# Optimization experiments

Hardware: AMD Instinct MI355X
Metric: run time of the kernel (lower is better)

Reference implementation:

```python
import jax, jax.numpy as jnp
import numpy as np

B, LQ, LK, D = 4, 2048, 2048, 1024
H = 16  # num_heads == num_kv_heads (only runnable config of the source module)
HD = D // H  # 64


def setup_inputs() -> dict:
    key = jax.random.key(0)
    ks = jax.random.split(key, 4)
    std = 0.02
    return {
        "x": jax.random.normal(ks[0], (B, LQ, D), dtype=jnp.float32),
        "text_input": jax.random.normal(ks[1], (B, LK, D), dtype=jnp.float32),
        "Wq": jax.random.normal(ks[2], (D, D), dtype=jnp.float32) * std,
        "bq": jnp.zeros((D,), dtype=jnp.float32),
        "Wkv": jax.random.normal(ks[3], (D, 2 * D), dtype=jnp.float32) * std,
        "bkv": jnp.zeros((2 * D,), dtype=jnp.float32),
    }


def reference(x, text_input, Wq, bq, Wkv, bkv):
    b, lq, d = x.shape
    lk = text_input.shape[1]
    # projections
    Q = x @ Wq + bq                       # [b, lq, d]
    KV = text_input @ Wkv + bkv           # [b, lk, 2d]
    K, V = jnp.split(KV, 2, axis=-1)      # [b, lk, d] each
    # split heads (num_kv_heads == num_heads, so repeat_interleave is identity)
    Q = Q.reshape(b, lq, H, HD)
    K = K.reshape(b, lk, H, HD)
    V = V.reshape(b, lk, H, HD)
    # scaled dot-product attention
    scale = 1.0 / jnp.sqrt(jnp.asarray(HD, dtype=Q.dtype))
    scores = jnp.einsum("bqhd,bkhd->bhqk", Q, K) * scale  # [b, H, lq, lk]
    attn = jax.nn.softmax(scores, axis=-1)
    out = jnp.einsum("bhqk,bkhd->bqhd", attn, V)          # [b, lq, H, HD]
    # dropout p=0.0 (eval) -> identity
    return out.reshape(b, lq, d)
```

## Files before the change

### kernel.cpp

```cpp
#include <hip/hip_runtime.h>
#include <hip/hip_bf16.h>


typedef unsigned short u16;
typedef unsigned int u32;

typedef __attribute__((ext_vector_type(8))) __bf16 bf16x8;
typedef __attribute__((ext_vector_type(2))) _Float16 f16x2;
typedef __attribute__((ext_vector_type(8))) _Float16 f16x8;
typedef __attribute__((ext_vector_type(4))) float f32x4;
typedef __attribute__((ext_vector_type(16))) float f32x16;
typedef __attribute__((ext_vector_type(4))) float f4;
typedef __attribute__((ext_vector_type(4))) unsigned short u16x4;

#define DEVI __device__ __forceinline__

DEVI u16 f2b(float f) {
  u32 u = __float_as_uint(f);
  return (u16)((u + 0x7fffu + ((u >> 16) & 1u)) >> 16);
}

DEVI u16 f2h(float f) {
  _Float16 h = (_Float16)f;
  return __builtin_bit_cast(u16, h);
}

DEVI f16x2 pk_f16(float a, float b) {
  return __builtin_bit_cast(f16x2, __builtin_amdgcn_cvt_pkrtz(a, b));
}

DEVI void gld_lds16(void* lds, const void* g) {
  __builtin_amdgcn_global_load_lds(
      (const __attribute__((address_space(1))) u32*)g,
      (__attribute__((address_space(3))) u32*)lds, 16, 0, 0);
}

__global__ __launch_bounds__(256) void k_prep(
    const float* __restrict__ x, const float* __restrict__ text,
    const float* __restrict__ Wq, const float* __restrict__ Wkv,
    u16* __restrict__ XB, u16* __restrict__ TB,
    u16* __restrict__ WQT, u16* __restrict__ WKVT) {
  __shared__ float tile[32][33];
  const int bid = blockIdx.x, tid = threadIdx.x;
  if (bid < 4096) {
    const float* in = (bid < 2048) ? x : text;
    u16* out = (bid < 2048) ? XB : TB;
    const int cb = (bid < 2048) ? bid : bid - 2048;
#pragma unroll
    for (int it = 0; it < 4; it++) {
      int i = cb * 256 + tid + it * 524288;
      f4 v = ((const f4*)in)[i];
      u16x4 o;
      o.x = f2b(v.x); o.y = f2b(v.y); o.z = f2b(v.z); o.w = f2b(v.w);
      ((u16x4*)out)[i] = o;
    }
  } else {
    const float* in;
    u16* out;
    int N, bx, by;
    if (bid < 5120) {
      int b2 = bid - 4096; in = Wq; out = WQT; N = 1024; bx = b2 & 31; by = b2 >> 5;
    } else {
      int b2 = bid - 5120; in = Wkv; out = WKVT; N = 2048; bx = b2 & 63; by = b2 >> 6;
    }
    const int K = 1024;
    const int n0 = bx * 32, k0 = by * 32;
    const int tx = tid & 31, ty = tid >> 5;
#pragma unroll
    for (int j = 0; j < 32; j += 8)
      tile[ty + j][tx] = in[(size_t)(k0 + ty + j) * N + n0 + tx];
    __syncthreads();
#pragma unroll
    for (int j = 0; j < 32; j += 8)
      out[(size_t)(n0 + ty + j) * K + k0 + tx] = f2b(tile[tx][ty + j]);
  }
}

__global__ __launch_bounds__(256) void k_gemm(
    const u16* __restrict__ XB, const u16* __restrict__ TB,
    const u16* __restrict__ WQT, const u16* __restrict__ WKVT,
    const float* __restrict__ bq, const float* __restrict__ bkv,
    u16* __restrict__ QG, u16* __restrict__ KG, u16* __restrict__ VG) {
  __shared__ alignas(16) char As[2][8192];
  __shared__ alignas(16) char Bs[2][8192];
  const int bid0 = blockIdx.x;
  const int bid = (bid0 & 7) * 192 + (bid0 >> 3);
  const int tid = threadIdx.x;
  const int w = tid >> 6, l = tid & 63;
  const int wr = w >> 1, wc = w & 1;

  const bool isQ = bid < 512;
  int nb, mb;
  const u16 *Aptr, *Bptr;
  const float* bias;
  if (isQ) {
    nb = bid & 7; mb = bid >> 3; Aptr = XB; Bptr = WQT; bias = bq;
  } else {
    int b2 = bid - 512; nb = b2 & 15; mb = b2 >> 4; Aptr = TB; Bptr = WKVT; bias = bkv;
  }
  const int m0 = mb << 7, n0 = nb << 7;

  u32 soff[2], doff[2];
#pragma unroll
  for (int i = 0; i < 2; i++) {
    u32 o = (u32)(i * 4096 + tid * 16);
    u32 row = o >> 6;
    soff[i] = row * 2048 + ((o & 63) ^ ((row & 3) << 4));
    doff[i] = o;
  }
  const char* Aorig = (const char*)Aptr + (size_t)m0 * 2048;
  const char* Borig = (const char*)Bptr + (size_t)n0 * 2048;

  f32x16 acc[2][2];
#pragma unroll
  for (int i = 0; i < 2; i++)
#pragma unroll
    for (int j = 0; j < 2; j++)
#pragma unroll
      for (int e = 0; e < 16; e++) acc[i][j][e] = 0.f;

  const u32 x3 = (u32)(l & 3);
  const u32 hi5 = (u32)(l >> 5);
  const u32 arow0 = (u32)(wr * 64 + (l & 31)) * 64;
  const u32 brow0 = (u32)(wc * 64 + (l & 31)) * 64;

#pragma unroll
  for (int i = 0; i < 2; i++) {
    gld_lds16(&As[0][doff[i]], Aorig + soff[i]);
    gld_lds16(&Bs[0][doff[i]], Borig + soff[i]);
  }
  __syncthreads();
  int buf = 0;
  for (int kt = 0; kt < 32; kt++) {
    if (kt < 31) {
#pragma unroll
      for (int i = 0; i < 2; i++) {
        gld_lds16(&As[buf ^ 1][doff[i]], Aorig + (u32)(kt + 1) * 64 + soff[i]);
        gld_lds16(&Bs[buf ^ 1][doff[i]], Borig + (u32)(kt + 1) * 64 + soff[i]);
      }
    }
    bf16x8 af[2][2], bfr[2][2];
#pragma unroll
    for (int i = 0; i < 2; i++)
#pragma unroll
      for (int h = 0; h < 2; h++) {
        const u32 co = (((u32)(2 * h) + hi5) ^ x3) << 4;
        af[i][h] = *(const bf16x8*)&As[buf][arow0 + (u32)i * 2048 + co];
        bfr[i][h] = *(const bf16x8*)&Bs[buf][brow0 + (u32)i * 2048 + co];
      }
#pragma unroll
    for (int i = 0; i < 2; i++)
#pragma unroll
      for (int j = 0; j < 2; j++)
#pragma unroll
        for (int h = 0; h < 2; h++)
          acc[i][j] = __builtin_amdgcn_mfma_f32_32x32x16_bf16(af[i][h], bfr[j][h], acc[i][j], 0, 0, 0);
    __syncthreads();
    buf ^= 1;
  }

#pragma unroll
  for (int i = 0; i < 2; i++)
#pragma unroll
    for (int j = 0; j < 2; j++) {
      const int n = n0 + wc * 64 + j * 32 + (l & 31);
      const float bv = bias[n];
#pragma unroll
      for (int rg = 0; rg < 4; rg++) {
        const int mbase = m0 + wr * 64 + i * 32 + rg * 8 + ((l >> 5) << 2);
        const int bb = mbase >> 11;
        const int mrow = mbase & 2047;
        float a0 = acc[i][j][rg * 4 + 0] + bv;
        float a1 = acc[i][j][rg * 4 + 1] + bv;
        float a2 = acc[i][j][rg * 4 + 2] + bv;
        float a3 = acc[i][j][rg * 4 + 3] + bv;
        if (isQ) {
          const int h = n >> 6, hd = n & 63;
          u16* dst = QG + ((((size_t)bb * 16 + h) * 2048 + mrow) << 6) + hd;
          dst[0] = f2b(a0 * 0.18033688011112042f);
          dst[64] = f2b(a1 * 0.18033688011112042f);
          dst[128] = f2b(a2 * 0.18033688011112042f);
          dst[192] = f2b(a3 * 0.18033688011112042f);
        } else if (n < 1024) {
          const int h = n >> 6, d = n & 63;
          char* base = (char*)KG + ((((size_t)bb * 16 + h) * 2048 + mrow) << 7);
          float av[4] = {a0, a1, a2, a3};
#pragma unroll
          for (int r = 0; r < 4; r++) {
            u32 off = (u32)r * 128 + (((u32)d * 2) ^ (((u32)(mrow + r) & 7) << 4));
            *(u16*)(base + off) = f2b(av[r]);
          }
        } else {
          const int nn = n - 1024;
          const int h = nn >> 6, hd = nn & 63;
          u16x4 pk;
          pk.x = f2h(a0); pk.y = f2h(a1); pk.z = f2h(a2); pk.w = f2h(a3);
          char* base = (char*)VG + (((size_t)bb * 16 + h) << 18);
          u32 off = ((u32)(mrow >> 6) << 13) + (((u32)(mrow >> 5) & 1) << 12) +
                    ((u32)(hd >> 4) << 10) + (((u32)(mrow >> 2) & 3) << 8) +
                    ((u32)(hd & 15) << 4) + (((u32)(mrow >> 4) & 1) << 3);
          *(u16x4*)(base + off) = pk;
        }
      }
    }
}

__global__ __launch_bounds__(256) void k_attn(
    const u16* __restrict__ QG, const u16* __restrict__ KG, const u16* __restrict__ VG,
    float* __restrict__ out) {
  __shared__ alignas(16) char Ks[2][8192];
  __shared__ alignas(16) char Vs[2][8192];
  const int tid = threadIdx.x, w = tid >> 6, l = tid & 63;
  const int g = l >> 4, q = l & 15;
  const int bid = blockIdx.x;
  const int orig = (bid & 7) * 128 + (bid >> 3);
  const int qt = orig & 15;
  const int hh = (orig >> 4) & 15;
  const int b = orig >> 8;
  const size_t bh = (size_t)b * 16 + hh;

  const int qrowA = qt * 128 + w * 16 + q;
  const int qrowB = qrowA + 64;

  const u16* QpA = QG + ((bh * 2048 + (size_t)qrowA) << 6) + (g << 3);
  const u16* QpB = QG + ((bh * 2048 + (size_t)qrowB) << 6) + (g << 3);
  const bf16x8 qf0a = *(const bf16x8*)QpA;
  const bf16x8 qf1a = *(const bf16x8*)(QpA + 32);
  const bf16x8 qf0b = *(const bf16x8*)QpB;
  const bf16x8 qf1b = *(const bf16x8*)(QpB + 32);

  const char* Kbase = (const char*)KG + (bh << 18);
  const char* Vbase = (const char*)VG + (bh << 18);

  f32x4 lsA = (f32x4){0.f, 0.f, 0.f, 0.f};
  f32x4 lsB = (f32x4){0.f, 0.f, 0.f, 0.f};
  f32x4 oa[4], ob4[4];
#pragma unroll
  for (int c = 0; c < 4; c++) {
    oa[c] = (f32x4){0.f, 0.f, 0.f, 0.f};
    ob4[c] = (f32x4){0.f, 0.f, 0.f, 0.f};
  }
  f16x8 ones8;
#pragma unroll
  for (int e = 0; e < 8; e++) ones8[e] = (_Float16)1.0f;

  gld_lds16(&Ks[0][tid * 16], Kbase + tid * 16);
  gld_lds16(&Ks[0][4096 + tid * 16], Kbase + 4096 + tid * 16);
  gld_lds16(&Vs[0][tid * 16], Vbase + tid * 16);
  gld_lds16(&Vs[0][4096 + tid * 16], Vbase + 4096 + tid * 16);
  __syncthreads();

  const u32 ksw = ((u32)(l & 7)) << 4;
  const u32 kro = ((u32)q) << 7;
  const u32 kin = ((u32)g) << 4;

  auto body = [&](int BUF, int kb) {
    if (kb < 31) {
      const char* kp = Kbase + (size_t)(kb + 1) * 8192 + tid * 16;
      const char* vp = Vbase + (size_t)(kb + 1) * 8192 + tid * 16;
      gld_lds16(&Ks[BUF ^ 1][tid * 16], kp);
      gld_lds16(&Ks[BUF ^ 1][4096 + tid * 16], kp + 4096);
      gld_lds16(&Vs[BUF ^ 1][tid * 16], vp);
      gld_lds16(&Vs[BUF ^ 1][4096 + tid * 16], vp + 4096);
    }
    f32x4 sa[4], sb[4];
    __builtin_amdgcn_s_setprio(1);
#pragma unroll
    for (int t = 0; t < 4; t++) {
      const char* kr = &Ks[BUF][kro + (u32)t * 2048];
      bf16x8 kf0 = *(const bf16x8*)(kr + (kin ^ ksw));
      bf16x8 kf1 = *(const bf16x8*)(kr + ((kin + 64) ^ ksw));
      f32x4 z = (f32x4){0.f, 0.f, 0.f, 0.f};
      sa[t] = __builtin_amdgcn_mfma_f32_16x16x32_bf16(kf0, qf0a, z, 0, 0, 0);
      sa[t] = __builtin_amdgcn_mfma_f32_16x16x32_bf16(kf1, qf1a, sa[t], 0, 0, 0);
      sb[t] = __builtin_amdgcn_mfma_f32_16x16x32_bf16(kf0, qf0b, z, 0, 0, 0);
      sb[t] = __builtin_amdgcn_mfma_f32_16x16x32_bf16(kf1, qf1b, sb[t], 0, 0, 0);
    }
    __builtin_amdgcn_s_setprio(0);

    float pA[4][4], pB[4][4];
#pragma unroll
    for (int t = 0; t < 4; t++)
#pragma unroll
      for (int r = 0; r < 4; r++) {
        pA[t][r] = __builtin_amdgcn_exp2f(sa[t][r]);
        pB[t][r] = __builtin_amdgcn_exp2f(sb[t][r]);
      }

    __builtin_amdgcn_s_setprio(1);
#pragma unroll
    for (int u = 0; u < 2; u++) {
      f16x2 a0 = pk_f16(pA[2 * u][0], pA[2 * u][1]);
      f16x2 a1 = pk_f16(pA[2 * u][2], pA[2 * u][3]);
      f16x2 a2 = pk_f16(pA[2 * u + 1][0], pA[2 * u + 1][1]);
      f16x2 a3 = pk_f16(pA[2 * u + 1][2], pA[2 * u + 1][3]);
      f16x8 pfa;
      pfa[0] = a0.x; pfa[1] = a0.y; pfa[2] = a1.x; pfa[3] = a1.y;
      pfa[4] = a2.x; pfa[5] = a2.y; pfa[6] = a3.x; pfa[7] = a3.y;
      f16x2 b0 = pk_f16(pB[2 * u][0], pB[2 * u][1]);
      f16x2 b1 = pk_f16(pB[2 * u][2], pB[2 * u][3]);
      f16x2 b2 = pk_f16(pB[2 * u + 1][0], pB[2 * u + 1][1]);
      f16x2 b3 = pk_f16(pB[2 * u + 1][2], pB[2 * u + 1][3]);
      f16x8 pfb;
      pfb[0] = b0.x; pfb[1] = b0.y; pfb[2] = b1.x; pfb[3] = b1.y;
      pfb[4] = b2.x; pfb[5] = b2.y; pfb[6] = b3.x; pfb[7] = b3.y;
      lsA = __builtin_amdgcn_mfma_f32_16x16x32_f16(ones8, pfa, lsA, 0, 0, 0);
      lsB = __builtin_amdgcn_mfma_f32_16x16x32_f16(ones8, pfb, lsB, 0, 0, 0);
#pragma unroll
      for (int c = 0; c < 4; c++) {
        f16x8 vf = *(const f16x8*)&Vs[BUF][(u32)u * 4096 + (u32)c * 1024 + (u32)l * 16];
        oa[c] = __builtin_amdgcn_mfma_f32_16x16x32_f16(vf, pfa, oa[c], 0, 0, 0);
        ob4[c] = __builtin_amdgcn_mfma_f32_16x16x32_f16(vf, pfb, ob4[c], 0, 0, 0);
      }
    }
    __builtin_amdgcn_s_setprio(0);
    __syncthreads();
  };

  for (int kb2 = 0; kb2 < 16; kb2++) {
    body(0, 2 * kb2);
    body(1, 2 * kb2 + 1);
  }

  const float invA = 1.0f / lsA.x;
  const float invB = 1.0f / lsB.x;
  float* obA = out + ((size_t)b * 2048 + (size_t)qrowA) * 1024 + hh * 64;
  float* obB = out + ((size_t)b * 2048 + (size_t)qrowB) * 1024 + hh * 64;
#pragma unroll
  for (int c = 0; c < 4; c++) {
    f32x4 va = oa[c] * invA;
    f32x4 vb2 = ob4[c] * invB;
    *(f32x4*)(obA + c * 16 + g * 4) = va;
    *(f32x4*)(obB + c * 16 + g * 4) = vb2;
  }
}

extern "C" void kernel_launch(void* const* d_in, const int* in_sizes, int n_in,
                              void* d_out, int out_size, void* d_ws, size_t ws_size,
                              hipStream_t stream) {
  const float* x = (const float*)d_in[0];
  const float* text = (const float*)d_in[1];
  const float* Wq = (const float*)d_in[2];
  const float* bq = (const float*)d_in[3];
  const float* Wkv = (const float*)d_in[4];
  const float* bkv = (const float*)d_in[5];
  float* out = (float*)d_out;
  char* ws = (char*)d_ws;

  const size_t MiB = 1u << 20;
  u16* XB = (u16*)(ws + 0 * MiB);
  u16* TB = (u16*)(ws + 16 * MiB);
  u16* WQT = (u16*)(ws + 32 * MiB);
  u16* WKVT = (u16*)(ws + 34 * MiB);
  u16* QG = (u16*)(ws + 38 * MiB);
  u16* KG = (u16*)(ws + 54 * MiB);
  u16* VG = (u16*)(ws + 70 * MiB);

  k_prep<<<7168, 256, 0, stream>>>(x, text, Wq, Wkv, XB, TB, WQT, WKVT);
  k_gemm<<<1536, 256, 0, stream>>>(XB, TB, WQT, WKVT, bq, bkv, QG, KG, VG);
  k_attn<<<1024, 256, 0, stream>>>(QG, KG, VG, out);
}
```

Before: 176.0 us.

## Fuse fp32-to-bf16 activation conversion into projection GEMM A-tile loads

```diff
diff --git a/kernel.cpp b/kernel.cpp
--- a/kernel.cpp
+++ b/kernel.cpp
@@ -12,6 +12,7 @@
 typedef __attribute__((ext_vector_type(16))) float f32x16;
 typedef __attribute__((ext_vector_type(4))) float f4;
 typedef __attribute__((ext_vector_type(4))) unsigned short u16x4;
+typedef __attribute__((ext_vector_type(4))) unsigned int u32x4;
 
 #define DEVI __device__ __forceinline__
 
@@ -27,6 +28,12 @@
 
 DEVI f16x2 pk_f16(float a, float b) {
   return __builtin_bit_cast(f16x2, __builtin_amdgcn_cvt_pkrtz(a, b));
+}
+
+DEVI u32 cvt_pk_bf16(float a, float b) {
+  u32 r;
+  asm("v_cvt_pk_bf16_f32 %0, %1, %2" : "=v"(r) : "v"(a), "v"(b));
+  return r;
 }
 
 DEVI void gld_lds16(void* lds, const void* g) {
@@ -36,48 +43,32 @@
 }
 
 __global__ __launch_bounds__(256) void k_prep(
-    const float* __restrict__ x, const float* __restrict__ text,
     const float* __restrict__ Wq, const float* __restrict__ Wkv,
-    u16* __restrict__ XB, u16* __restrict__ TB,
     u16* __restrict__ WQT, u16* __restrict__ WKVT) {
   __shared__ float tile[32][33];
   const int bid = blockIdx.x, tid = threadIdx.x;
-  if (bid < 4096) {
-    const float* in = (bid < 2048) ? x : text;
-    u16* out = (bid < 2048) ? XB : TB;
-    const int cb = (bid < 2048) ? bid : bid - 2048;
-#pragma unroll
-    for (int it = 0; it < 4; it++) {
-      int i = cb * 256 + tid + it * 524288;
-      f4 v = ((const f4*)in)[i];
-      u16x4 o;
-      o.x = f2b(v.x); o.y = f2b(v.y); o.z = f2b(v.z); o.w = f2b(v.w);
-      ((u16x4*)out)[i] = o;
-    }
+  const float* in;
+  u16* out;
+  int N, bx, by;
+  if (bid < 1024) {
+    in = Wq; out = WQT; N = 1024; bx = bid & 31; by = bid >> 5;
   } else {
-    const float* in;
-    u16* out;
-    int N, bx, by;
-    if (bid < 5120) {
-      int b2 = bid - 4096; in = Wq; out = WQT; N = 1024; bx = b2 & 31; by = b2 >> 5;
-    } else {
-      int b2 = bid - 5120; in = Wkv; out = WKVT; N = 2048; bx = b2 & 63; by = b2 >> 6;
-    }
-    const int K = 1024;
-    const int n0 = bx * 32, k0 = by * 32;
-    const int tx = tid & 31, ty = tid >> 5;
-#pragma unroll
-    for (int j = 0; j < 32; j += 8)
-      tile[ty + j][tx] = in[(size_t)(k0 + ty + j) * N + n0 + tx];
-    __syncthreads();
-#pragma unroll
-    for (int j = 0; j < 32; j += 8)
-      out[(size_t)(n0 + ty + j) * K + k0 + tx] = f2b(tile[tx][ty + j]);
-  }
+    int b2 = bid - 1024; in = Wkv; out = WKVT; N = 2048; bx = b2 & 63; by = b2 >> 6;
+  }
+  const int K = 1024;
+  const int n0 = bx * 32, k0 = by * 32;
+  const int tx = tid & 31, ty = tid >> 5;
+#pragma unroll
+  for (int j = 0; j < 32; j += 8)
+    tile[ty + j][tx] = in[(size_t)(k0 + ty + j) * N + n0 + tx];
+  __syncthreads();
+#pragma unroll
+  for (int j = 0; j < 32; j += 8)
+    out[(size_t)(n0 + ty + j) * K + k0 + tx] = f2b(tile[tx][ty + j]);
 }
 
 __global__ __launch_bounds__(256) void k_gemm(
-    const u16* __restrict__ XB, const u16* __restrict__ TB,
+    const float* __restrict__ X, const float* __restrict__ TXT,
     const u16* __restrict__ WQT, const u16* __restrict__ WKVT,
     const float* __restrict__ bq, const float* __restrict__ bkv,
     u16* __restrict__ QG, u16* __restrict__ KG, u16* __restrict__ VG) {
@@ -91,24 +82,27 @@
 
   const bool isQ = bid < 512;
   int nb, mb;
-  const u16 *Aptr, *Bptr;
+  const float* Af32;
+  const u16* Bptr;
   const float* bias;
   if (isQ) {
-    nb = bid & 7; mb = bid >> 3; Aptr = XB; Bptr = WQT; bias = bq;
+    nb = bid & 7; mb = bid >> 3; Af32 = X; Bptr = WQT; bias = bq;
   } else {
-    int b2 = bid - 512; nb = b2 & 15; mb = b2 >> 4; Aptr = TB; Bptr = WKVT; bias = bkv;
+    int b2 = bid - 512; nb = b2 & 15; mb = b2 >> 4; Af32 = TXT; Bptr = WKVT; bias = bkv;
   }
   const int m0 = mb << 7, n0 = nb << 7;
 
-  u32 soff[2], doff[2];
+  u32 doff[2], bsoff[2], fsoff[2];
 #pragma unroll
   for (int i = 0; i < 2; i++) {
     u32 o = (u32)(i * 4096 + tid * 16);
     u32 row = o >> 6;
-    soff[i] = row * 2048 + ((o & 63) ^ ((row & 3) << 4));
+    u32 csw = (o & 63) ^ ((row & 3) << 4);
     doff[i] = o;
-  }
-  const char* Aorig = (const char*)Aptr + (size_t)m0 * 2048;
+    bsoff[i] = row * 2048 + csw;
+    fsoff[i] = row * 4096 + 2 * csw;
+  }
+  const char* Abase = (const char*)Af32 + (size_t)m0 * 4096;
   const char* Borig = (const char*)Bptr + (size_t)n0 * 2048;
 
   f32x16 acc[2][2];
@@ -126,17 +120,27 @@
 
 #pragma unroll
   for (int i = 0; i < 2; i++) {
-    gld_lds16(&As[0][doff[i]], Aorig + soff[i]);
-    gld_lds16(&Bs[0][doff[i]], Borig + soff[i]);
+    gld_lds16(&Bs[0][doff[i]], Borig + bsoff[i]);
+    f4 a0 = *(const f4*)(Abase + fsoff[i]);
+    f4 a1 = *(const f4*)(Abase + fsoff[i] + 16);
+    u32x4 pk;
+    pk.x = cvt_pk_bf16(a0.x, a0.y);
+    pk.y = cvt_pk_bf16(a0.z, a0.w);
+    pk.z = cvt_pk_bf16(a1.x, a1.y);
+    pk.w = cvt_pk_bf16(a1.z, a1.w);
+    *(u32x4*)&As[0][doff[i]] = pk;
   }
   __syncthreads();
+
   int buf = 0;
   for (int kt = 0; kt < 32; kt++) {
+    f4 a0[2], a1[2];
     if (kt < 31) {
 #pragma unroll
       for (int i = 0; i < 2; i++) {
-        gld_lds16(&As[buf ^ 1][doff[i]], Aorig + (u32)(kt + 1) * 64 + soff[i]);
-        gld_lds16(&Bs[buf ^ 1][doff[i]], Borig + (u32)(kt + 1) * 64 + soff[i]);
+        gld_lds16(&Bs[buf ^ 1][doff[i]], Borig + (u32)(kt + 1) * 64 + bsoff[i]);
+        a0[i] = *(const f4*)(Abase + (u32)(kt + 1) * 128 + fsoff[i]);
+        a1[i] = *(const f4*)(Abase + (u32)(kt + 1) * 128 + fsoff[i] + 16);
       }
     }
     bf16x8 af[2][2], bfr[2][2];
@@ -155,6 +159,17 @@
 #pragma unroll
         for (int h = 0; h < 2; h++)
           acc[i][j] = __builtin_amdgcn_mfma_f32_32x32x16_bf16(af[i][h], bfr[j][h], acc[i][j], 0, 0, 0);
+    if (kt < 31) {
+#pragma unroll
+      for (int i = 0; i < 2; i++) {
+        u32x4 pk;
+        pk.x = cvt_pk_bf16(a0[i].x, a0[i].y);
+        pk.y = cvt_pk_bf16(a0[i].z, a0[i].w);
+        pk.z = cvt_pk_bf16(a1[i].x, a1[i].y);
+        pk.w = cvt_pk_bf16(a1[i].z, a1[i].w);
+        *(u32x4*)&As[buf ^ 1][doff[i]] = pk;
+      }
+    }
     __syncthreads();
     buf ^= 1;
   }
@@ -348,15 +363,13 @@
   char* ws = (char*)d_ws;
 
   const size_t MiB = 1u << 20;
-  u16* XB = (u16*)(ws + 0 * MiB);
-  u16* TB = (u16*)(ws + 16 * MiB);
-  u16* WQT = (u16*)(ws + 32 * MiB);
-  u16* WKVT = (u16*)(ws + 34 * MiB);
-  u16* QG = (u16*)(ws + 38 * MiB);
-  u16* KG = (u16*)(ws + 54 * MiB);
-  u16* VG = (u16*)(ws + 70 * MiB);
-
-  k_prep<<<7168, 256, 0, stream>>>(x, text, Wq, Wkv, XB, TB, WQT, WKVT);
-  k_gemm<<<1536, 256, 0, stream>>>(XB, TB, WQT, WKVT, bq, bkv, QG, KG, VG);
+  u16* WQT = (u16*)(ws + 0 * MiB);
+  u16* WKVT = (u16*)(ws + 2 * MiB);
+  u16* QG = (u16*)(ws + 6 * MiB);
+  u16* KG = (u16*)(ws + 22 * MiB);
+  u16* VG = (u16*)(ws + 38 * MiB);
+
+  k_prep<<<3072, 256, 0, stream>>>(Wq, Wkv, WQT, WKVT);
+  k_gemm<<<1536, 256, 0, stream>>>(x, text, WQT, WKVT, bq, bkv, QG, KG, VG);
   k_attn<<<1024, 256, 0, stream>>>(QG, KG, VG, out);
 }
```

Result: faster. 169.8 us (-3.6%).
